# Performance work log

Measured on AMD Instinct MI355X. Metric: run time of the kernel, lower is better.

The kernel has to match this reference:

```python
import jax, jax.numpy as jnp
import numpy as np

N = 20000      # nodes
K = 32         # avg degree
E = N * K      # edges
H = 128        # num_hidden
NV = 128       # num_V
NE = 128       # num_E
NH = 4         # num_heads (hard-coded in module)
D = H // NH    # per-head dim


def setup_inputs() -> dict:
    key = jax.random.key(0)
    ks = jax.random.split(key, 16)
    w = lambda k, shape: jax.random.normal(k, shape, jnp.float32) * 0.02
    return {
        "h_V": jax.random.normal(ks[0], (N, NV), jnp.float32),
        "h_E": jax.random.normal(ks[1], (E, NE), jnp.float32),
        "edge_idx": jax.random.randint(ks[2], (2, E), 0, N, dtype=jnp.int64),
        # W_V: Linear(num_E, num_hidden) + GELU
        "Wv_w": w(ks[3], (H, NE)), "Wv_b": jnp.zeros((H,), jnp.float32),
        # Bias MLP: Linear(2*num_V+num_E, H) -> ReLU -> Linear(H, H) -> ReLU -> Linear(H, NH)
        "B1_w": w(ks[4], (H, 2 * NV + NE)), "B1_b": jnp.zeros((H,), jnp.float32),
        "B2_w": w(ks[5], (H, H)), "B2_b": jnp.zeros((H,), jnp.float32),
        "B3_w": w(ks[6], (NH, H)), "B3_b": jnp.zeros((NH,), jnp.float32),
        # W_O: Linear(H, num_V, bias=False); gate: Linear(H, num_V)
        "Wo_w": w(ks[7], (NV, H)),
        "gate_w": w(ks[8], (NV, H)), "gate_b": jnp.zeros((NV,), jnp.float32),
    }


def reference(h_V, h_E, edge_idx, Wv_w, Wv_b, B1_w, B1_b, B2_w, B2_b, B3_w, B3_b, Wo_w, gate_w, gate_b):
    src = edge_idx[0]
    dst = edge_idx[1]
    num_nodes = h_V.shape[0]

    # per-edge attention logits via small MLP on [h_V[src], h_E, h_V[dst]]
    cat = jnp.concatenate([h_V[src], h_E, h_V[dst]], axis=-1)          # [E, 2*NV+NE]
    x = jax.nn.relu(cat @ B1_w.T + B1_b)
    x = jax.nn.relu(x @ B2_w.T + B2_b)
    logits = (x @ B3_w.T + B3_b) / np.float32(np.sqrt(D))              # [E, NH]

    # per-edge values
    V = jax.nn.gelu(h_E @ Wv_w.T + Wv_b, approximate=False)           # [E, H]
    V = V.reshape(-1, NH, D)                                           # [E, NH, D]

    # scatter_softmax over edges grouped by src node
    m = jax.ops.segment_max(logits, src, num_segments=num_nodes)       # [N, NH]
    ex = jnp.exp(logits - m[src])                                      # [E, NH]
    denom = jax.ops.segment_sum(ex, src, num_segments=num_nodes)      # [N, NH]
    attend = ex / denom[src]                                           # [E, NH]

    # weighted scatter-sum aggregation
    agg = jax.ops.segment_sum(attend[:, :, None] * V, src, num_segments=num_nodes)
    agg = agg.reshape(num_nodes, -1)                                   # [N, H]

    h_V_gate = jax.nn.sigmoid(agg @ gate_w.T + gate_b)                 # [N, NV]
    dh = (agg @ Wo_w.T) * h_V_gate                                     # [N, NV]
    return h_V + dh
```

## Files before the change

### kernel.cpp

```cpp
#include <hip/hip_runtime.h>
#include <math.h>

typedef __attribute__((ext_vector_type(8))) short bf16x8;
typedef __attribute__((ext_vector_type(4))) float f32x4;
typedef unsigned short u16;

__device__ __forceinline__ short f2bf(float x) {
  union { float f; unsigned u; } c; c.f = x;
  unsigned u = c.u;
  u += 0x7fffu + ((u >> 16) & 1u);
  return (short)(u >> 16);
}
__device__ __forceinline__ float bf2f(u16 b) {
  union { unsigned u; float f; } c; c.u = ((unsigned)b) << 16; return c.f;
}
__device__ __forceinline__ unsigned pack2(float a, float b) {
  return ((unsigned)(u16)f2bf(a)) | (((unsigned)(u16)f2bf(b)) << 16);
}
__device__ __forceinline__ unsigned cvtpk(float lo, float hi) {
  unsigned r;
  asm("v_cvt_pk_bf16_f32 %0, %1, %2" : "=v"(r) : "v"(lo), "v"(hi));
  return r;
}
__device__ __forceinline__ u16 f2bf1(float x) {
  return (u16)cvtpk(x, x);
}
__device__ __forceinline__ float bfu_lo(unsigned v) {
  union { unsigned u; float f; } c; c.u = v << 16; return c.f;
}
__device__ __forceinline__ float bfu_hi(unsigned v) {
  union { unsigned u; float f; } c; c.u = v & 0xffff0000u; return c.f;
}
__device__ __forceinline__ float fast_erf(float x) {
  float ax = fabsf(x);
  float p = 1.f + ax * (0.278393f + ax * (0.230389f + ax * (0.000972f + ax * 0.078108f)));
  p = p * p; p = p * p;
  float y = 1.f - __frcp_rn(p);
  return copysignf(y, x);
}
__device__ __forceinline__ float gelu1(float x) {
  return 0.5f * x * (1.0f + fast_erf(x * 0.70710678118654752f));
}
__device__ __forceinline__ void gload16(const void* g, void* l) {
  __builtin_amdgcn_global_load_lds(
      (const __attribute__((address_space(1))) void*)g,
      (__attribute__((address_space(3))) void*)l, 16, 0, 0);
}

__global__ void detect_kernel(const unsigned* __restrict__ idx32, int* __restrict__ flag) {
  __shared__ int anyNZ;
  if (threadIdx.x == 0) anyNZ = 0;
  __syncthreads();
  unsigned v = idx32[threadIdx.x * 2 + 1];
  if (v != 0u) atomicOr(&anyNZ, 1);
  __syncthreads();
  if (threadIdx.x == 0) *flag = (anyNZ == 0) ? 1 : 0;
}

__global__ void convert_count_kernel(const void* __restrict__ in, int* __restrict__ s32,
                                     const int* __restrict__ flag, int* __restrict__ cnt,
                                     int E) {
  int i = blockIdx.x * 256 + threadIdx.x;
  if (i >= 2 * E) return;
  int f = *flag;
  int v = f ? (int)((const long long*)in)[i] : ((const int*)in)[i];
  s32[i] = v;
  if (i < E) atomicAdd(&cnt[v], 1);
}

__global__ void __launch_bounds__(1024)
scan_kernel(const int* __restrict__ cnt, int* __restrict__ offs, int n) {
  __shared__ int sp[1024];
  int t = threadIdx.x;
  int chunk = (n + 1023) / 1024;
  int begin = t * chunk;
  int end = begin + chunk; if (end > n) end = n; if (begin > n) begin = n;
  int s = 0;
  for (int i = begin; i < end; ++i) s += cnt[i];
  sp[t] = s;
  __syncthreads();
  for (int o = 1; o < 1024; o <<= 1) {
    int v = (t >= o) ? sp[t - o] : 0;
    __syncthreads();
    sp[t] += v;
    __syncthreads();
  }
  int run = (t == 0) ? 0 : sp[t - 1];
  for (int i = begin; i < end; ++i) { offs[i] = run; run += cnt[i]; }
  if (t == 0) offs[n] = sp[1023];
}

__global__ void scatter_kernel(const int* __restrict__ src, const int* __restrict__ offs,
                               int* __restrict__ cur, int* __restrict__ order, int E) {
  int i = blockIdx.x * 256 + threadIdx.x;
  if (i >= E) return;
  int s = src[i];
  int p = offs[s] + atomicAdd(&cur[s], 1);
  order[p] = i;
}

__global__ void wcvt_kernel(const float* __restrict__ B1, const float* __restrict__ B2,
                            const float* __restrict__ B3, const float* __restrict__ Wv,
                            const float* __restrict__ Wo, const float* __restrict__ Wg,
                            short* __restrict__ o) {
  int i = blockIdx.x * 256 + threadIdx.x;
  if (i >= 115200) return;
  float val; int dst;
  if (i < 49152) {
    int row = i / 384, k = i % 384;
    val = B1[i];
    int c = k >> 5, s = (k >> 3) & 3, e = k & 7;
    dst = c * 4096 + row * 32 + ((s ^ ((row >> 1) & 3)) << 3) + e;
  } else if (i < 65536) {
    int j = i - 49152; int row = j >> 7, k = j & 127;
    val = B2[j];
    int c = k >> 5, s = (k >> 3) & 3, e = k & 7;
    dst = 49152 + c * 4096 + row * 32 + ((s ^ ((row >> 1) & 3)) << 3) + e;
  } else if (i < 66048) { val = B3[i - 65536]; dst = i; }
  else if (i < 82432) {
    int j = i - 66048; int row = j >> 7, k = j & 127;
    val = Wv[j];
    int c = k >> 5, s = (k >> 3) & 3, e = k & 7;
    dst = 66048 + c * 4096 + row * 32 + ((s ^ ((row >> 1) & 3)) << 3) + e;
  }
  else if (i < 98816)  { val = Wo[i - 82432]; dst = i; }
  else                 { val = Wg[i - 98816]; dst = i; }
  o[dst] = f2bf(val);
}

__global__ void cvtbf_kernel(const float* __restrict__ in, u16* __restrict__ out, long n8) {
  long i = (long)blockIdx.x * blockDim.x + threadIdx.x;
  long stride = (long)gridDim.x * blockDim.x;
  for (; i < n8; i += stride) {
    long b = i * 8;
    float4 a = *(const float4*)(in + b);
    float4 c = *(const float4*)(in + b + 4);
    uint4 u;
    u.x = pack2(a.x, a.y); u.y = pack2(a.z, a.w);
    u.z = pack2(c.x, c.y); u.w = pack2(c.z, c.w);
    *(uint4*)(out + b) = u;
  }
}

__global__ void __launch_bounds__(256, 4)
edge_kernel(const u16* __restrict__ hVb, const float* __restrict__ hE,
            const int* __restrict__ src, const int* __restrict__ dst,
            u16* __restrict__ Vout,
            const short* __restrict__ W1, const float* __restrict__ b1,
            const short* __restrict__ W2, const float* __restrict__ b2,
            const short* __restrict__ W3b, const float* __restrict__ b3,
            const short* __restrict__ Wv, const float* __restrict__ bv,
            float* __restrict__ logits, int E) {
  __shared__ u16 sEH[64 * 128];
  __shared__ u16 sW[2][4096];
  __shared__ float sPart[64][4][2];

  const int t = threadIdx.x;
  const int eBase = blockIdx.x * 64;
  const int lane = t & 63;
  const int wid = t >> 6;
  const int wrow = (wid >> 1) * 32;
  const int wcol = (wid & 1) * 64;
  const int lrow = lane & 15;
  const int kgrp = lane >> 4;

  auto STAGE = [&](const short* cp, int buf) {
#pragma unroll
    for (int i = 0; i < 2; ++i) {
      int L = t + i * 256;
      gload16(cp + L * 8, &sW[buf][L * 8]);
    }
  };

  STAGE(Wv, 0);

#pragma unroll
  for (int i = 0; i < 4; ++i) {
    int u = t + i * 256;
    int row = u >> 4, sg = u & 15;
    const float* p = hE + (size_t)min(eBase + row, E - 1) * 128 + sg * 8;
    float4 f0 = *(const float4*)p;
    float4 f1 = *(const float4*)(p + 4);
    uint4 cv;
    cv.x = cvtpk(f0.x, f0.y); cv.y = cvtpk(f0.z, f0.w);
    cv.z = cvtpk(f1.x, f1.y); cv.w = cvtpk(f1.z, f1.w);
    *(uint4*)&sEH[row * 128 + ((sg ^ (row & 15)) * 8)] = cv;
  }

  int rS[2], rD[2];
#pragma unroll
  for (int mi = 0; mi < 2; ++mi) {
    int e = min(eBase + wrow + mi * 16 + lrow, E - 1);
    rS[mi] = src[e];
    rD[mi] = dst[e];
  }
  asm volatile("s_waitcnt vmcnt(0)" ::: "memory");
  __syncthreads();

  f32x4 acc[2][4];
  auto ZACC = [&]() {
#pragma unroll
    for (int mi = 0; mi < 2; ++mi)
#pragma unroll
      for (int nf = 0; nf < 4; ++nf)
#pragma unroll
        for (int q = 0; q < 4; ++q) acc[mi][nf][q] = 0.f;
  };
  auto LDSA = [&](int kk, bf16x8* a) {
#pragma unroll
    for (int mi = 0; mi < 2; ++mi) {
      int row = wrow + mi * 16 + lrow;
      int seg = (kk >> 3) ^ (row & 15);
      a[mi] = *(const bf16x8*)&sEH[row * 128 + seg * 8];
    }
  };
  auto STEP = [&](int buf, const short* nextCp, const bf16x8* a) {
    if (nextCp) STAGE(nextCp, buf ^ 1);
    bf16x8 b[4];
#pragma unroll
    for (int nf = 0; nf < 4; ++nf) {
      int row = wcol + nf * 16 + lrow;
      int seg = kgrp ^ ((row >> 1) & 3);
      b[nf] = *(const bf16x8*)&sW[buf][row * 32 + seg * 8];
    }
#pragma unroll
    for (int nf = 0; nf < 4; ++nf)
#pragma unroll
      for (int mi = 0; mi < 2; ++mi)
        acc[mi][nf] = __builtin_amdgcn_mfma_f32_16x16x32_bf16(a[mi], b[nf], acc[mi][nf], 0, 0, 0);
    if (nextCp) asm volatile("s_waitcnt vmcnt(0)" ::: "memory");
    __syncthreads();
  };
  auto STEPG = [&](int buf, const short* nextCp, const int* r, int c4) {
    bf16x8 a[2];
    const int kk = c4 * 32 + kgrp * 8;
#pragma unroll
    for (int mi = 0; mi < 2; ++mi)
      a[mi] = *(const bf16x8*)(hVb + (size_t)r[mi] * 128 + kk);
    STEP(buf, nextCp, a);
  };

  ZACC();
#pragma unroll
  for (int c = 0; c < 4; ++c) {
    bf16x8 a[2];
    LDSA(c * 32 + kgrp * 8, a);
    const short* nxt = (c < 3) ? (Wv + (c + 1) * 4096) : (W1 + 4 * 4096);
    STEP(c & 1, nxt, a);
  }
  unsigned vpk[2][4][2];
  {
    float bvc[4];
#pragma unroll
    for (int nf = 0; nf < 4; ++nf) bvc[nf] = bv[wcol + nf * 16 + lrow];
#pragma unroll
    for (int mi = 0; mi < 2; ++mi)
#pragma unroll
      for (int nf = 0; nf < 4; ++nf) {
        vpk[mi][nf][0] = cvtpk(acc[mi][nf][0] + bvc[nf], acc[mi][nf][1] + bvc[nf]);
        vpk[mi][nf][1] = cvtpk(acc[mi][nf][2] + bvc[nf], acc[mi][nf][3] + bvc[nf]);
      }
  }

  ZACC();
#pragma unroll
  for (int c = 0; c < 4; ++c) {
    bf16x8 a[2];
    LDSA(c * 32 + kgrp * 8, a);
    const short* nxt = (c < 3) ? (W1 + (5 + c) * 4096) : W1;
    STEP(c & 1, nxt, a);
  }
  STEPG(0, W1 + 1 * 4096, rS, 0);
  STEPG(1, W1 + 2 * 4096, rS, 1);
  STEPG(0, W1 + 3 * 4096, rS, 2);
  STEPG(1, W1 + 8 * 4096, rS, 3);
  STEPG(0, W1 + 9 * 4096, rD, 0);
  STEPG(1, W1 + 10 * 4096, rD, 1);
  STEPG(0, W1 + 11 * 4096, rD, 2);
  STEPG(1, W2, rD, 3);

  {
    float b1c[4];
#pragma unroll
    for (int nf = 0; nf < 4; ++nf) b1c[nf] = b1[wcol + nf * 16 + lrow];
#pragma unroll
    for (int mi = 0; mi < 2; ++mi)
#pragma unroll
      for (int nf = 0; nf < 4; ++nf)
#pragma unroll
        for (int q = 0; q < 4; ++q) {
          int row = wrow + mi * 16 + kgrp * 4 + q;
          int col = wcol + nf * 16 + lrow;
          int seg = (col >> 3) ^ (row & 15);
          sEH[row * 128 + seg * 8 + (col & 7)] =
              f2bf1(fmaxf(acc[mi][nf][q] + b1c[nf], 0.f));
        }
  }
  __syncthreads();

  ZACC();
#pragma unroll
  for (int c = 0; c < 4; ++c) {
    bf16x8 a[2];
    LDSA(c * 32 + kgrp * 8, a);
    const short* nxt = (c < 3) ? (W2 + (c + 1) * 4096) : nullptr;
    STEP(c & 1, nxt, a);
  }
  {
    float b2c[4], w3v[4][4];
#pragma unroll
    for (int nf = 0; nf < 4; ++nf) {
      int col = wcol + nf * 16 + lrow;
      b2c[nf] = b2[col];
#pragma unroll
      for (int h = 0; h < 4; ++h) w3v[h][nf] = bf2f((u16)W3b[h * 128 + col]);
    }
#pragma unroll
    for (int mi = 0; mi < 2; ++mi)
#pragma unroll
      for (int q = 0; q < 4; ++q) {
        float p0 = 0.f, p1 = 0.f, p2 = 0.f, p3 = 0.f;
#pragma unroll
        for (int nf = 0; nf < 4; ++nf) {
          float x = fmaxf(acc[mi][nf][q] + b2c[nf], 0.f);
          p0 += x * w3v[0][nf]; p1 += x * w3v[1][nf];
          p2 += x * w3v[2][nf]; p3 += x * w3v[3][nf];
        }
#pragma unroll
        for (int o = 1; o < 16; o <<= 1) {
          p0 += __shfl_xor(p0, o); p1 += __shfl_xor(p1, o);
          p2 += __shfl_xor(p2, o); p3 += __shfl_xor(p3, o);
        }
        if (lrow < 4) {
          float pw = (lrow == 0) ? p0 : (lrow == 1) ? p1 : (lrow == 2) ? p2 : p3;
          sPart[wrow + mi * 16 + kgrp * 4 + q][lrow][wid & 1] = pw;
        }
      }
  }
  __syncthreads();
  if (t < 64) {
    int e = eBase + t;
    if (e < E) {
      float4 lg;
      lg.x = (sPart[t][0][0] + sPart[t][0][1] + b3[0]) * 0.17677669529663687f;
      lg.y = (sPart[t][1][0] + sPart[t][1][1] + b3[1]) * 0.17677669529663687f;
      lg.z = (sPart[t][2][0] + sPart[t][2][1] + b3[2]) * 0.17677669529663687f;
      lg.w = (sPart[t][3][0] + sPart[t][3][1] + b3[3]) * 0.17677669529663687f;
      *(float4*)(logits + (size_t)e * 4) = lg;
    }
  }

#pragma unroll
  for (int mi = 0; mi < 2; ++mi)
#pragma unroll
    for (int nf = 0; nf < 4; ++nf)
#pragma unroll
      for (int p = 0; p < 2; ++p) {
        float x0 = bfu_lo(vpk[mi][nf][p]);
        float x1 = bfu_hi(vpk[mi][nf][p]);
        int col = wcol + nf * 16 + lrow;
        int row0 = wrow + mi * 16 + kgrp * 4 + p * 2;
        int seg0 = (col >> 3) ^ (row0 & 15);
        int seg1 = (col >> 3) ^ ((row0 + 1) & 15);
        sEH[row0 * 128 + seg0 * 8 + (col & 7)] = f2bf1(gelu1(x0));
        sEH[(row0 + 1) * 128 + seg1 * 8 + (col & 7)] = f2bf1(gelu1(x1));
      }
  __syncthreads();
#pragma unroll
  for (int i = 0; i < 4; ++i) {
    int u = t + i * 256;
    int row = u >> 4, g16 = u & 15;
    int seg = g16 ^ (row & 15);
    uint4 v = *(const uint4*)&sEH[row * 128 + seg * 8];
    int e = eBase + row;
    if (e < E) *(uint4*)(Vout + (size_t)e * 128 + g16 * 8) = v;
  }
}

__global__ void __launch_bounds__(256)
nm_kernel(const float* __restrict__ logits, const int* __restrict__ offs,
          const int* __restrict__ order, float* __restrict__ attw,
          float* __restrict__ inv, int nN) {
  const int wid = threadIdx.x >> 6, lane = threadIdx.x & 63;
  const int nW = gridDim.x * 4;
  for (int v = blockIdx.x * 4 + wid; v < nN; v += nW) {
    const int base = offs[v];
    const int deg = offs[v + 1] - base;
    float m0 = -3e38f, m1 = -3e38f, m2 = -3e38f, m3 = -3e38f;
    for (int i = lane; i < deg; i += 64) {
      int e = order[base + i];
      float4 l = *(const float4*)(logits + (size_t)e * 4);
      m0 = fmaxf(m0, l.x); m1 = fmaxf(m1, l.y);
      m2 = fmaxf(m2, l.z); m3 = fmaxf(m3, l.w);
    }
#pragma unroll
    for (int o = 32; o > 0; o >>= 1) {
      m0 = fmaxf(m0, __shfl_xor(m0, o)); m1 = fmaxf(m1, __shfl_xor(m1, o));
      m2 = fmaxf(m2, __shfl_xor(m2, o)); m3 = fmaxf(m3, __shfl_xor(m3, o));
    }
    float d0 = 0.f, d1 = 0.f, d2 = 0.f, d3 = 0.f;
    for (int i = lane; i < deg; i += 64) {
      int e = order[base + i];
      float4 l = *(const float4*)(logits + (size_t)e * 4);
      float4 ex;
      ex.x = __expf(l.x - m0); ex.y = __expf(l.y - m1);
      ex.z = __expf(l.z - m2); ex.w = __expf(l.w - m3);
      *(float4*)(attw + (size_t)e * 4) = ex;
      d0 += ex.x; d1 += ex.y; d2 += ex.z; d3 += ex.w;
    }
#pragma unroll
    for (int o = 32; o > 0; o >>= 1) {
      d0 += __shfl_xor(d0, o); d1 += __shfl_xor(d1, o);
      d2 += __shfl_xor(d2, o); d3 += __shfl_xor(d3, o);
    }
    if (lane < 4) {
      float dv = (lane == 0) ? d0 : (lane == 1) ? d1 : (lane == 2) ? d2 : d3;
      inv[(size_t)v * 4 + lane] = (dv > 0.f) ? 1.f / dv : 0.f;
    }
  }
}

__device__ __forceinline__ float dot8(const float* ag, uint4 w) {
  unsigned wr[4] = {w.x, w.y, w.z, w.w};
  float s = 0.f;
#pragma unroll
  for (int q = 0; q < 4; ++q) {
    s += ag[2 * q]     * bf2f((u16)(wr[q] & 0xffffu));
    s += ag[2 * q + 1] * bf2f((u16)(wr[q] >> 16));
  }
  return s;
}

__global__ void __launch_bounds__(256, 2)
agg_kernel(const float* __restrict__ hV, const float* __restrict__ attw,
           const float* __restrict__ inv, const u16* __restrict__ V,
           const int* __restrict__ offs, const int* __restrict__ order,
           const short* __restrict__ Wob, const short* __restrict__ Wgb,
           const float* __restrict__ gb, float* __restrict__ out, int nN) {
  __shared__ u16 sW[2][16384];
  __shared__ float sAgg[4][132];
  const int t = threadIdx.x;
#pragma unroll
  for (int i = 0; i < 8; ++i) {
    int idx = t + i * 256;
    int row = idx >> 4, k16 = idx & 15;
    int di = row * 128 + ((k16 ^ (row & 15)) * 8);
    *(uint4*)&sW[0][di] = ((const uint4*)Wob)[idx];
    *(uint4*)&sW[1][di] = ((const uint4*)Wgb)[idx];
  }
  __syncthreads();
  const int wid = t >> 6, lane = t & 63;
  const int dgrp = lane & 15, egrp = lane >> 4, h = dgrp >> 2;
  const int j0 = lane, j1 = lane + 64;
  const int s0 = (j0 & 15), s1 = (j1 & 15);
  for (int v = blockIdx.x * 4 + wid; v < nN; v += gridDim.x * 4) {
    const int base = offs[v], deg = offs[v + 1] - base;
    float a[8];
#pragma unroll
    for (int q = 0; q < 8; ++q) a[q] = 0.f;
    for (int i = egrp; i < deg; i += 4) {
      int e = order[base + i];
      float w = attw[(size_t)e * 4 + h];
      bf16x8 vv = *(const bf16x8*)(V + (size_t)e * 128 + dgrp * 8);
#pragma unroll
      for (int q = 0; q < 8; ++q) a[q] += w * bf2f((u16)vv[q]);
    }
#pragma unroll
    for (int q = 0; q < 8; ++q) {
      a[q] += __shfl_xor(a[q], 16);
      a[q] += __shfl_xor(a[q], 32);
    }
    if (egrp == 0) {
      float innv = inv[(size_t)v * 4 + h];
#pragma unroll
      for (int q = 0; q < 8; ++q) sAgg[wid][dgrp * 8 + q] = a[q] * innv;
    }
    asm volatile("s_waitcnt lgkmcnt(0)" ::: "memory");
    __builtin_amdgcn_wave_barrier();
    float o0 = 0.f, o1 = 0.f, g0 = 0.f, g1 = 0.f;
#pragma unroll 4
    for (int k = 0; k < 128; k += 8) {
      float a8[8];
#pragma unroll
      for (int q = 0; q < 8; ++q) a8[q] = sAgg[wid][k + q];
      int k16 = k >> 3;
      uint4 wo0 = *(const uint4*)&sW[0][j0 * 128 + ((k16 ^ s0) * 8)];
      uint4 wo1 = *(const uint4*)&sW[0][j1 * 128 + ((k16 ^ s1) * 8)];
      uint4 wg0 = *(const uint4*)&sW[1][j0 * 128 + ((k16 ^ s0) * 8)];
      uint4 wg1 = *(const uint4*)&sW[1][j1 * 128 + ((k16 ^ s1) * 8)];
      o0 += dot8(a8, wo0); o1 += dot8(a8, wo1);
      g0 += dot8(a8, wg0); g1 += dot8(a8, wg1);
    }
    float gg0 = 1.f / (1.f + __expf(-(g0 + gb[j0])));
    float gg1 = 1.f / (1.f + __expf(-(g1 + gb[j1])));
    out[(size_t)v * 128 + j0] = hV[(size_t)v * 128 + j0] + o0 * gg0;
    out[(size_t)v * 128 + j1] = hV[(size_t)v * 128 + j1] + o1 * gg1;
    asm volatile("s_waitcnt lgkmcnt(0)" ::: "memory");
    __builtin_amdgcn_wave_barrier();
  }
}

__global__ void fb_kernel(const float* __restrict__ hV, float* __restrict__ out, int n) {
  int i = blockIdx.x * 256 + threadIdx.x;
  if (i < n) out[i] = hV[i] + 0.5f;
}

extern "C" void kernel_launch(void* const* d_in, const int* in_sizes, int n_in,
                              void* d_out, int out_size, void* d_ws, size_t ws_size,
                              hipStream_t stream) {
  const float* hV   = (const float*)d_in[0];
  const float* hE   = (const float*)d_in[1];
  const void*  eidx = d_in[2];
  const float* WvW  = (const float*)d_in[3];
  const float* WvB  = (const float*)d_in[4];
  const float* B1w  = (const float*)d_in[5];
  const float* B1b  = (const float*)d_in[6];
  const float* B2w  = (const float*)d_in[7];
  const float* B2b  = (const float*)d_in[8];
  const float* B3w  = (const float*)d_in[9];
  const float* B3b  = (const float*)d_in[10];
  const float* WoW  = (const float*)d_in[11];
  const float* GW   = (const float*)d_in[12];
  const float* GB   = (const float*)d_in[13];

  const int Nn = in_sizes[0] / 128;
  const int E  = in_sizes[1] / 128;
  if (Nn <= 0 || E <= 0) return;

  char* ws = (char*)d_ws;
  size_t off = 0;
  auto alloc = [&](size_t b) { size_t o = off; off += (b + 255) & ~(size_t)255; return o; };
  const size_t o_idx   = alloc((size_t)2 * E * 4);
  const size_t o_cnt   = alloc((size_t)(Nn + 1) * 4);
  const size_t o_offs  = alloc((size_t)(Nn + 1) * 4);
  const size_t o_cur   = alloc((size_t)Nn * 4);
  const size_t o_order = alloc((size_t)E * 4);
  const size_t o_flag  = alloc(256);
  const size_t o_log   = alloc((size_t)E * 16);
  const size_t o_attw  = alloc((size_t)E * 16);
  const size_t o_inv   = alloc((size_t)Nn * 16);
  const size_t o_V     = alloc((size_t)E * 256);
  const size_t o_hVb   = alloc((size_t)Nn * 256);
  const size_t o_wbf   = alloc((size_t)115200 * 2);

  if (off > ws_size) {
    fb_kernel<<<(out_size + 255) / 256, 256, 0, stream>>>(hV, (float*)d_out, out_size);
    return;
  }

  int*   idx32  = (int*)(ws + o_idx);
  int*   cnt    = (int*)(ws + o_cnt);
  int*   offsP  = (int*)(ws + o_offs);
  int*   cur    = (int*)(ws + o_cur);
  int*   order  = (int*)(ws + o_order);
  int*   flag   = (int*)(ws + o_flag);
  float* logits = (float*)(ws + o_log);
  float* attw   = (float*)(ws + o_attw);
  float* invd   = (float*)(ws + o_inv);
  u16*   Vb     = (u16*)(ws + o_V);
  u16*   hVb    = (u16*)(ws + o_hVb);
  short* wbf    = (short*)(ws + o_wbf);

  short* W1b = wbf;
  short* W2b = wbf + 49152;
  short* W3b = wbf + 65536;
  short* Wvb = wbf + 66048;
  short* Wob = wbf + 82432;
  short* Wgb = wbf + 98816;

  const int* src = idx32;
  const int* dst = idx32 + E;

  detect_kernel<<<1, 256, 0, stream>>>((const unsigned*)eidx, flag);
  hipMemsetAsync(cnt, 0, (size_t)(Nn + 1) * 4, stream);
  hipMemsetAsync(cur, 0, (size_t)Nn * 4, stream);
  convert_count_kernel<<<(2 * E + 255) / 256, 256, 0, stream>>>(eidx, idx32, flag, cnt, E);
  scan_kernel<<<1, 1024, 0, stream>>>(cnt, offsP, Nn);
  scatter_kernel<<<(E + 255) / 256, 256, 0, stream>>>(src, offsP, cur, order, E);
  wcvt_kernel<<<(115200 + 255) / 256, 256, 0, stream>>>(B1w, B2w, B3w, WvW, WoW, GW, wbf);
  cvtbf_kernel<<<512, 256, 0, stream>>>(hV, hVb, (long)Nn * 16);

  edge_kernel<<<(E + 63) / 64, 256, 0, stream>>>(
      hVb, hE, src, dst, Vb, W1b, B1b, W2b, B2b, W3b, B3b, Wvb, WvB, logits, E);

  nm_kernel<<<2048, 256, 0, stream>>>(logits, offsP, order, attw, invd, Nn);

  agg_kernel<<<512, 256, 0, stream>>>(
      hV, attw, invd, Vb, offsP, order, Wob, Wgb, GB, (float*)d_out, Nn);
}
```

Baseline: 512.2 us.

## Enlarge edge tile to 128 rows and fold softmax normalization into aggregation

The edge MLP kernel now processes 128 edges per block instead of 64, so each wave computes a 64x64 output tile. This doubles reuse of each staged weight chunk and halves the number of weight loads and barriers per edge, at the cost of more registers, more LDS and lower occupancy (launch bounds drop from 4 to 3). The separate segment-max/exp/denominator kernel is removed; the aggregation kernel computes the per-node max and the exp-sum itself. This avoids writing and re-reading the attention-weight and inverse-denominator arrays and saves a kernel launch, but each node's logits are now read twice inside the aggregation kernel.

New measurement: 577.3 us. 12.7% more time.

```diff
diff --git a/kernel.cpp b/kernel.cpp
--- a/kernel.cpp
+++ b/kernel.cpp
@@ -142,7 +142,7 @@
   }
 }
 
-__global__ void __launch_bounds__(256, 4)
+__global__ void __launch_bounds__(256, 3)
 edge_kernel(const u16* __restrict__ hVb, const float* __restrict__ hE,
             const int* __restrict__ src, const int* __restrict__ dst,
             u16* __restrict__ Vout,
@@ -151,15 +151,15 @@
             const short* __restrict__ W3b, const float* __restrict__ b3,
             const short* __restrict__ Wv, const float* __restrict__ bv,
             float* __restrict__ logits, int E) {
-  __shared__ u16 sEH[64 * 128];
+  __shared__ u16 sEH[128 * 128];
   __shared__ u16 sW[2][4096];
-  __shared__ float sPart[64][4][2];
+  __shared__ float sPart[128][4][2];
 
   const int t = threadIdx.x;
-  const int eBase = blockIdx.x * 64;
+  const int eBase = blockIdx.x * 128;
   const int lane = t & 63;
   const int wid = t >> 6;
-  const int wrow = (wid >> 1) * 32;
+  const int wrow = (wid >> 1) * 64;
   const int wcol = (wid & 1) * 64;
   const int lrow = lane & 15;
   const int kgrp = lane >> 4;
@@ -175,7 +175,7 @@
   STAGE(Wv, 0);
 
 #pragma unroll
-  for (int i = 0; i < 4; ++i) {
+  for (int i = 0; i < 8; ++i) {
     int u = t + i * 256;
     int row = u >> 4, sg = u & 15;
     const float* p = hE + (size_t)min(eBase + row, E - 1) * 128 + sg * 8;
@@ -187,9 +187,9 @@
     *(uint4*)&sEH[row * 128 + ((sg ^ (row & 15)) * 8)] = cv;
   }
 
-  int rS[2], rD[2];
-#pragma unroll
-  for (int mi = 0; mi < 2; ++mi) {
+  int rS[4], rD[4];
+#pragma unroll
+  for (int mi = 0; mi < 4; ++mi) {
     int e = min(eBase + wrow + mi * 16 + lrow, E - 1);
     rS[mi] = src[e];
     rD[mi] = dst[e];
@@ -197,10 +197,10 @@
   asm volatile("s_waitcnt vmcnt(0)" ::: "memory");
   __syncthreads();
 
-  f32x4 acc[2][4];
+  f32x4 acc[4][4];
   auto ZACC = [&]() {
 #pragma unroll
-    for (int mi = 0; mi < 2; ++mi)
+    for (int mi = 0; mi < 4; ++mi)
 #pragma unroll
       for (int nf = 0; nf < 4; ++nf)
 #pragma unroll
@@ -208,7 +208,7 @@
   };
   auto LDSA = [&](int kk, bf16x8* a) {
 #pragma unroll
-    for (int mi = 0; mi < 2; ++mi) {
+    for (int mi = 0; mi < 4; ++mi) {
       int row = wrow + mi * 16 + lrow;
       int seg = (kk >> 3) ^ (row & 15);
       a[mi] = *(const bf16x8*)&sEH[row * 128 + seg * 8];
@@ -226,16 +226,16 @@
 #pragma unroll
     for (int nf = 0; nf < 4; ++nf)
 #pragma unroll
-      for (int mi = 0; mi < 2; ++mi)
+      for (int mi = 0; mi < 4; ++mi)
         acc[mi][nf] = __builtin_amdgcn_mfma_f32_16x16x32_bf16(a[mi], b[nf], acc[mi][nf], 0, 0, 0);
     if (nextCp) asm volatile("s_waitcnt vmcnt(0)" ::: "memory");
     __syncthreads();
   };
   auto STEPG = [&](int buf, const short* nextCp, const int* r, int c4) {
-    bf16x8 a[2];
+    bf16x8 a[4];
     const int kk = c4 * 32 + kgrp * 8;
 #pragma unroll
-    for (int mi = 0; mi < 2; ++mi)
+    for (int mi = 0; mi < 4; ++mi)
       a[mi] = *(const bf16x8*)(hVb + (size_t)r[mi] * 128 + kk);
     STEP(buf, nextCp, a);
   };
@@ -243,18 +243,18 @@
   ZACC();
 #pragma unroll
   for (int c = 0; c < 4; ++c) {
-    bf16x8 a[2];
+    bf16x8 a[4];
     LDSA(c * 32 + kgrp * 8, a);
     const short* nxt = (c < 3) ? (Wv + (c + 1) * 4096) : (W1 + 4 * 4096);
     STEP(c & 1, nxt, a);
   }
-  unsigned vpk[2][4][2];
+  unsigned vpk[4][4][2];
   {
     float bvc[4];
 #pragma unroll
     for (int nf = 0; nf < 4; ++nf) bvc[nf] = bv[wcol + nf * 16 + lrow];
 #pragma unroll
-    for (int mi = 0; mi < 2; ++mi)
+    for (int mi = 0; mi < 4; ++mi)
 #pragma unroll
       for (int nf = 0; nf < 4; ++nf) {
         vpk[mi][nf][0] = cvtpk(acc[mi][nf][0] + bvc[nf], acc[mi][nf][1] + bvc[nf]);
@@ -265,7 +265,7 @@
   ZACC();
 #pragma unroll
   for (int c = 0; c < 4; ++c) {
-    bf16x8 a[2];
+    bf16x8 a[4];
     LDSA(c * 32 + kgrp * 8, a);
     const short* nxt = (c < 3) ? (W1 + (5 + c) * 4096) : W1;
     STEP(c & 1, nxt, a);
@@ -284,7 +284,7 @@
 #pragma unroll
     for (int nf = 0; nf < 4; ++nf) b1c[nf] = b1[wcol + nf * 16 + lrow];
 #pragma unroll
-    for (int mi = 0; mi < 2; ++mi)
+    for (int mi = 0; mi < 4; ++mi)
 #pragma unroll
       for (int nf = 0; nf < 4; ++nf)
 #pragma unroll
@@ -301,7 +301,7 @@
   ZACC();
 #pragma unroll
   for (int c = 0; c < 4; ++c) {
-    bf16x8 a[2];
+    bf16x8 a[4];
     LDSA(c * 32 + kgrp * 8, a);
     const short* nxt = (c < 3) ? (W2 + (c + 1) * 4096) : nullptr;
     STEP(c & 1, nxt, a);
@@ -316,7 +316,7 @@
       for (int h = 0; h < 4; ++h) w3v[h][nf] = bf2f((u16)W3b[h * 128 + col]);
     }
 #pragma unroll
-    for (int mi = 0; mi < 2; ++mi)
+    for (int mi = 0; mi < 4; ++mi)
 #pragma unroll
       for (int q = 0; q < 4; ++q) {
         float p0 = 0.f, p1 = 0.f, p2 = 0.f, p3 = 0.f;
@@ -338,20 +338,17 @@
       }
   }
   __syncthreads();
-  if (t < 64) {
-    int e = eBase + t;
-    if (e < E) {
-      float4 lg;
-      lg.x = (sPart[t][0][0] + sPart[t][0][1] + b3[0]) * 0.17677669529663687f;
-      lg.y = (sPart[t][1][0] + sPart[t][1][1] + b3[1]) * 0.17677669529663687f;
-      lg.z = (sPart[t][2][0] + sPart[t][2][1] + b3[2]) * 0.17677669529663687f;
-      lg.w = (sPart[t][3][0] + sPart[t][3][1] + b3[3]) * 0.17677669529663687f;
-      *(float4*)(logits + (size_t)e * 4) = lg;
-    }
-  }
-
-#pragma unroll
-  for (int mi = 0; mi < 2; ++mi)
+#pragma unroll
+  for (int it = 0; it < 2; ++it) {
+    int item = t * 2 + it;
+    int r = item >> 2, h = item & 3;
+    float lg = (sPart[r][h][0] + sPart[r][h][1] + b3[h]) * 0.17677669529663687f;
+    int e = eBase + r;
+    if (e < E) logits[(size_t)e * 4 + h] = lg;
+  }
+
+#pragma unroll
+  for (int mi = 0; mi < 4; ++mi)
 #pragma unroll
     for (int nf = 0; nf < 4; ++nf)
 #pragma unroll
@@ -367,7 +364,7 @@
       }
   __syncthreads();
 #pragma unroll
-  for (int i = 0; i < 4; ++i) {
+  for (int i = 0; i < 8; ++i) {
     int u = t + i * 256;
     int row = u >> 4, g16 = u & 15;
     int seg = g16 ^ (row & 15);
@@ -377,49 +374,6 @@
   }
 }
 
-__global__ void __launch_bounds__(256)
-nm_kernel(const float* __restrict__ logits, const int* __restrict__ offs,
-          const int* __restrict__ order, float* __restrict__ attw,
-          float* __restrict__ inv, int nN) {
-  const int wid = threadIdx.x >> 6, lane = threadIdx.x & 63;
-  const int nW = gridDim.x * 4;
-  for (int v = blockIdx.x * 4 + wid; v < nN; v += nW) {
-    const int base = offs[v];
-    const int deg = offs[v + 1] - base;
-    float m0 = -3e38f, m1 = -3e38f, m2 = -3e38f, m3 = -3e38f;
-    for (int i = lane; i < deg; i += 64) {
-      int e = order[base + i];
-      float4 l = *(const float4*)(logits + (size_t)e * 4);
-      m0 = fmaxf(m0, l.x); m1 = fmaxf(m1, l.y);
-      m2 = fmaxf(m2, l.z); m3 = fmaxf(m3, l.w);
-    }
-#pragma unroll
-    for (int o = 32; o > 0; o >>= 1) {
-      m0 = fmaxf(m0, __shfl_xor(m0, o)); m1 = fmaxf(m1, __shfl_xor(m1, o));
-      m2 = fmaxf(m2, __shfl_xor(m2, o)); m3 = fmaxf(m3, __shfl_xor(m3, o));
-    }
-    float d0 = 0.f, d1 = 0.f, d2 = 0.f, d3 = 0.f;
-    for (int i = lane; i < deg; i += 64) {
-      int e = order[base + i];
-      float4 l = *(const float4*)(logits + (size_t)e * 4);
-      float4 ex;
-      ex.x = __expf(l.x - m0); ex.y = __expf(l.y - m1);
-      ex.z = __expf(l.z - m2); ex.w = __expf(l.w - m3);
-      *(float4*)(attw + (size_t)e * 4) = ex;
-      d0 += ex.x; d1 += ex.y; d2 += ex.z; d3 += ex.w;
-    }
-#pragma unroll
-    for (int o = 32; o > 0; o >>= 1) {
-      d0 += __shfl_xor(d0, o); d1 += __shfl_xor(d1, o);
-      d2 += __shfl_xor(d2, o); d3 += __shfl_xor(d3, o);
-    }
-    if (lane < 4) {
-      float dv = (lane == 0) ? d0 : (lane == 1) ? d1 : (lane == 2) ? d2 : d3;
-      inv[(size_t)v * 4 + lane] = (dv > 0.f) ? 1.f / dv : 0.f;
-    }
-  }
-}
-
 __device__ __forceinline__ float dot8(const float* ag, uint4 w) {
   unsigned wr[4] = {w.x, w.y, w.z, w.w};
   float s = 0.f;
@@ -432,8 +386,8 @@
 }
 
 __global__ void __launch_bounds__(256, 2)
-agg_kernel(const float* __restrict__ hV, const float* __restrict__ attw,
-           const float* __restrict__ inv, const u16* __restrict__ V,
+agg_kernel(const float* __restrict__ hV, const float* __restrict__ logits,
+           const u16* __restrict__ V,
            const int* __restrict__ offs, const int* __restrict__ order,
            const short* __restrict__ Wob, const short* __restrict__ Wgb,
            const float* __restrict__ gb, float* __restrict__ out, int nN) {
@@ -455,12 +409,21 @@
   const int s0 = (j0 & 15), s1 = (j1 & 15);
   for (int v = blockIdx.x * 4 + wid; v < nN; v += gridDim.x * 4) {
     const int base = offs[v], deg = offs[v + 1] - base;
-    float a[8];
-#pragma unroll
-    for (int q = 0; q < 8; ++q) a[q] = 0.f;
+    float m = -3e38f;
     for (int i = egrp; i < deg; i += 4) {
       int e = order[base + i];
-      float w = attw[(size_t)e * 4 + h];
+      m = fmaxf(m, logits[(size_t)e * 4 + h]);
+    }
+    m = fmaxf(m, __shfl_xor(m, 16));
+    m = fmaxf(m, __shfl_xor(m, 32));
+    float a[8];
+#pragma unroll
+    for (int q = 0; q < 8; ++q) a[q] = 0.f;
+    float dsum = 0.f;
+    for (int i = egrp; i < deg; i += 4) {
+      int e = order[base + i];
+      float w = __expf(logits[(size_t)e * 4 + h] - m);
+      dsum += w;
       bf16x8 vv = *(const bf16x8*)(V + (size_t)e * 128 + dgrp * 8);
 #pragma unroll
       for (int q = 0; q < 8; ++q) a[q] += w * bf2f((u16)vv[q]);
@@ -470,8 +433,10 @@
       a[q] += __shfl_xor(a[q], 16);
       a[q] += __shfl_xor(a[q], 32);
     }
+    dsum += __shfl_xor(dsum, 16);
+    dsum += __shfl_xor(dsum, 32);
+    float innv = (dsum > 0.f) ? __frcp_rn(dsum) : 0.f;
     if (egrp == 0) {
-      float innv = inv[(size_t)v * 4 + h];
 #pragma unroll
       for (int q = 0; q < 8; ++q) sAgg[wid][dgrp * 8 + q] = a[q] * innv;
     }
@@ -537,8 +502,6 @@
   const size_t o_order = alloc((size_t)E * 4);
   const size_t o_flag  = alloc(256);
   const size_t o_log   = alloc((size_t)E * 16);
-  const size_t o_attw  = alloc((size_t)E * 16);
-  const size_t o_inv   = alloc((size_t)Nn * 16);
   const size_t o_V     = alloc((size_t)E * 256);
   const size_t o_hVb   = alloc((size_t)Nn * 256);
   const size_t o_wbf   = alloc((size_t)115200 * 2);
@@ -555,8 +518,6 @@
   int*   order  = (int*)(ws + o_order);
   int*   flag   = (int*)(ws + o_flag);
   float* logits = (float*)(ws + o_log);
-  float* attw   = (float*)(ws + o_attw);
-  float* invd   = (float*)(ws + o_inv);
   u16*   Vb     = (u16*)(ws + o_V);
   u16*   hVb    = (u16*)(ws + o_hVb);
   short* wbf    = (short*)(ws + o_wbf);
@@ -580,11 +541,9 @@
   wcvt_kernel<<<(115200 + 255) / 256, 256, 0, stream>>>(B1w, B2w, B3w, WvW, WoW, GW, wbf);
   cvtbf_kernel<<<512, 256, 0, stream>>>(hV, hVb, (long)Nn * 16);
 
-  edge_kernel<<<(E + 63) / 64, 256, 0, stream>>>(
+  edge_kernel<<<(E + 127) / 128, 256, 0, stream>>>(
       hVb, hE, src, dst, Vb, W1b, B1b, W2b, B2b, W3b, B3b, Wvb, WvB, logits, E);
 
-  nm_kernel<<<2048, 256, 0, stream>>>(logits, offsP, order, attw, invd, Nn);
-
   agg_kernel<<<512, 256, 0, stream>>>(
-      hV, attw, invd, Vb, offsP, order, Wob, Wgb, GB, (float*)d_out, Nn);
-}
+      hV, logits, Vb, offsP, order, Wob, Wgb, GB, (float*)d_out, Nn);
+}
```
